# Kernel tuning notes

Measured on AMD Instinct MI355X. Metric: run time of the kernel, lower is better.

Reference implementation:

```python
import jax, jax.numpy as jnp
import numpy as np

B, C, LQ, D = 4096, 64, 32, 128
H = 192  # 1.5 * dim
MARGIN = 1.0
EPS = 1e-12


def l2norm(x):
    return x * jax.lax.rsqrt(jnp.maximum(jnp.sum(x * x, axis=1, keepdims=True), EPS))


def setup_inputs() -> dict:
    key = jax.random.key(0)
    ks = jax.random.split(key, 16)
    question_word_embs = jax.random.normal(ks[0], (B, LQ, D), jnp.float32)
    question_lengths = jax.random.randint(ks[1], (B,), 1, LQ + 1, jnp.int32)
    header_embs = jax.random.normal(ks[2], (B, C, D), jnp.float32)
    table_word_embs = jax.random.normal(ks[3], (B, C, D), jnp.float32)
    num_cols = jax.random.randint(ks[4], (B,), 1, C + 1, jnp.int32)
    masks = (jnp.arange(C)[None, :] < num_cols[:, None]).astype(jnp.float32)
    labels = (jax.random.uniform(ks[5], (B,)) < 0.5).astype(jnp.float32)
    # table_encoder_dense: Dense(1.5*dim, relu) -> Dense(dim, relu)
    W1 = jax.random.normal(ks[6], (2 * D, H), jnp.float32) / np.sqrt(2 * D)
    b1 = jnp.zeros((H,), jnp.float32)
    W2 = jax.random.normal(ks[7], (H, D), jnp.float32) / np.sqrt(H)
    b2 = jnp.zeros((D,), jnp.float32)
    # query LSTM(dim, activation='relu'): gate order i, f, c, o (Keras)
    Wx = jax.random.normal(ks[8], (D, 4 * D), jnp.float32) / np.sqrt(D)
    Wh = jax.random.normal(ks[9], (D, 4 * D), jnp.float32) / np.sqrt(D)
    b_lstm = jnp.zeros((4 * D,), jnp.float32)
    return dict(question_word_embs=question_word_embs, question_lengths=question_lengths,
                header_embs=header_embs, table_word_embs=table_word_embs,
                num_cols=num_cols, masks=masks, labels=labels,
                W1=W1, b1=b1, W2=W2, b2=b2, Wx=Wx, Wh=Wh, b_lstm=b_lstm)


def masked_lstm(x, lengths, Wx, Wh, b):
    # x: [B, L, D]; returns final hidden state at each row's true length
    xs = jnp.transpose(x, (1, 0, 2))  # [L, B, D]
    h0 = jnp.zeros((x.shape[0], D), x.dtype)
    c0 = jnp.zeros_like(h0)

    def step(carry, inp):
        h, c = carry
        t, x_t = inp
        z = x_t @ Wx + h @ Wh + b  # [B, 4D]
        i, f, g, o = jnp.split(z, 4, axis=1)
        i = jax.nn.sigmoid(i)
        f = jax.nn.sigmoid(f)
        g = jax.nn.relu(g)           # activation='relu'
        o = jax.nn.sigmoid(o)
        c_new = f * c + i * g
        h_new = o * jax.nn.relu(c_new)
        m = (t < lengths)[:, None].astype(x_t.dtype)
        return (m * h_new + (1 - m) * h, m * c_new + (1 - m) * c), None

    (h, _), _ = jax.lax.scan(step, (h0, c0), (jnp.arange(xs.shape[0]), xs))
    return h


def reference(question_word_embs, question_lengths, header_embs, table_word_embs,
              num_cols, masks, labels, W1, b1, W2, b2, Wx, Wh, b_lstm):
    # ---- table path ----
    flat = jnp.concatenate([header_embs.reshape(-1, D), table_word_embs.reshape(-1, D)], axis=1)  # [B*C, 2D]
    h = jax.nn.relu(flat @ W1 + b1)
    te = jax.nn.relu(h @ W2 + b2).reshape(B, C, D)
    te = te * masks[:, :, None]
    te = jnp.sum(te, axis=1) / num_cols.astype(jnp.float32)[:, None]
    te = l2norm(te)
    # ---- query path (ragged-word LSTM encoder) ----
    qe = masked_lstm(question_word_embs, question_lengths, Wx, Wh, b_lstm)
    qe = l2norm(qe)
    # ---- contrastive loss ----
    d = jnp.sum(jnp.square(qe - te), axis=1)
    d_sqrt = jnp.sqrt(d)
    loss = labels * d + (1.0 - labels) * jnp.square(jnp.maximum(0.0, MARGIN - d_sqrt))
    return 0.5 * jnp.mean(loss)
```

## Files before the change

### kernel.cpp

```cpp
#include <hip/hip_runtime.h>
#include <math.h>

#define B_  4096
#define C_  64
#define LQ_ 32
#define D_  128
#define H_  192

typedef __attribute__((ext_vector_type(8))) short bf16x8;
typedef __attribute__((ext_vector_type(4))) float f32x4;

#define KEEP(x) asm volatile("" : "+v"(x))

__device__ inline unsigned cvt_pk_bf16(float lo, float hi) {
    unsigned r;
    asm("v_cvt_pk_bf16_f32 %0, %1, %2" : "=v"(r) : "v"(lo), "v"(hi));
    return r;
}
__device__ inline short f2b(float x) { return (short)(cvt_pk_bf16(x, x) & 0xffff); }
__device__ inline float sigm(float x) { return 1.f / (1.f + __expf(-x)); }

__device__ inline void wg_barrier() {
    asm volatile("s_waitcnt lgkmcnt(0)" ::: "memory");
    __builtin_amdgcn_s_barrier();
    asm volatile("" ::: "memory");
}

__global__ __launch_bounds__(256) void prep_kernel(
    const float* __restrict__ W1, const float* __restrict__ W2,
    const float* __restrict__ Wx, const float* __restrict__ Wh,
    short* __restrict__ W1T, short* __restrict__ W2T, short* __restrict__ WTl)
{
    int idx = blockIdx.x * 256 + threadIdx.x;
    if (idx < 192 * 256) {
        int j = idx >> 8, k = idx & 255;
        W1T[idx] = f2b(W1[k * H_ + j]);
    }
    if (idx < 128 * 192) {
        int j = idx / 192, k = idx - j * 192;
        W2T[idx] = f2b(W2[k * D_ + j]);
    }
    if (idx < 512 * 256) {
        int p = idx >> 8, k = idx & 255;
        int w = p >> 6, g = (p >> 4) & 3, jj = p & 15;
        int jo = g * 128 + w * 16 + jj;
        float v = (k < 128) ? Wx[k * 512 + jo] : Wh[(k - 128) * 512 + jo];
        WTl[idx] = f2b(v);
    }
}

__global__ __launch_bounds__(256, 2)
void table_kernel(
    const float* __restrict__ header, const float* __restrict__ tword,
    const float* __restrict__ masks, const int* __restrict__ num_cols,
    const short* __restrict__ W1T, const float* __restrict__ b1,
    const short* __restrict__ W2T, const float* __restrict__ b2,
    float* __restrict__ te_out)
{
    const int bb0 = blockIdx.x * 4;
    const int tid = threadIdx.x;
    const int w   = tid >> 6;
    const int l   = tid & 63;
    const int lg  = l >> 4;
    const int ln  = l & 15;

    __shared__ __align__(16) float flat32[3][16 * 256];
    __shared__ __align__(16) short h_s[16 * 192];
    __shared__ float msk_s[4][64];
    __shared__ float ncol_s[4];
    __shared__ float csum_s[4][128];
    __shared__ float redq[2][4];

    bf16x8 bw1[3][8];
    float  bias1[3][4];
    #pragma unroll
    for (int ct = 0; ct < 3; ++ct) {
        int j = w * 48 + ct * 16 + ln;
        #pragma unroll
        for (int ks = 0; ks < 8; ++ks)
            bw1[ct][ks] = *(const bf16x8*)&W1T[j * 256 + ks * 32 + lg * 8];
        #pragma unroll
        for (int reg = 0; reg < 4; ++reg)
            bias1[ct][reg] = b1[w * 48 + ct * 16 + lg * 4 + reg];
    }
    #pragma unroll
    for (int ct = 0; ct < 3; ++ct) {
        #pragma unroll
        for (int ks = 0; ks < 8; ++ks) KEEP(bw1[ct][ks]);
        #pragma unroll
        for (int reg = 0; reg < 4; ++reg) KEEP(bias1[ct][reg]);
    }

    ((float*)msk_s)[tid] = masks[(size_t)bb0 * C_ + tid];
    if (tid < 4) ncol_s[tid] = (float)num_cols[bb0 + tid];

    auto stage_issue = [&](int cc, int buf) {
        int b    = bb0 + (cc >> 2);
        int row0 = (cc & 3) * 16;
        #pragma unroll
        for (int i = 0; i < 4; ++i) {
            int r = w * 4 + i;
            int p = ((l * 16) ^ ((r & 7) << 4)) >> 2;
            const float* srcp = (p < 128)
                ? header + ((size_t)b * C_ + row0 + r) * D_ + p
                : tword  + ((size_t)b * C_ + row0 + r) * D_ + (p - 128);
            __builtin_amdgcn_global_load_lds(
                (const __attribute__((address_space(1))) unsigned*)srcp,
                (__attribute__((address_space(3))) unsigned*)&flat32[buf][r * 256],
                16, 0, 0);
        }
    };

    stage_issue(0, 0);
    stage_issue(1, 1);
    __syncthreads();

    float csum[2][4] = {{0.f, 0.f, 0.f, 0.f}, {0.f, 0.f, 0.f, 0.f}};
    const int swz = (ln & 7) << 4;

    #pragma unroll 1
    for (int cc = 0; cc < 16; ++cc) {
        const int bi = cc >> 2;

        bf16x8 w2f[2][6];
        #pragma unroll
        for (int ct = 0; ct < 2; ++ct)
            #pragma unroll
            for (int ks = 0; ks < 6; ++ks)
                w2f[ct][ks] = *(const bf16x8*)&W2T[(w * 32 + ct * 16 + ln) * 192 + ks * 32 + lg * 8];
        float4 b2v[2];
        #pragma unroll
        for (int ct = 0; ct < 2; ++ct)
            b2v[ct] = *(const float4*)&b2[w * 32 + ct * 16 + lg * 4];
        if (cc + 2 < 16) stage_issue(cc + 2, (cc + 2) % 3);

        {
            const char* fb = (const char*)flat32[cc % 3] + ln * 1024;
            f32x4 acc[3];
            #pragma unroll
            for (int ct = 0; ct < 3; ++ct)
                acc[ct] = (f32x4){bias1[ct][0], bias1[ct][1], bias1[ct][2], bias1[ct][3]};
            #pragma unroll
            for (int ks = 0; ks < 8; ++ks) {
                int base = ks * 128 + lg * 32;
                f32x4 a0 = *(const f32x4*)(fb + ((base)      ^ swz));
                f32x4 a1 = *(const f32x4*)(fb + ((base + 16) ^ swz));
                unsigned uu[4];
                uu[0] = cvt_pk_bf16(a0[0], a0[1]);
                uu[1] = cvt_pk_bf16(a0[2], a0[3]);
                uu[2] = cvt_pk_bf16(a1[0], a1[1]);
                uu[3] = cvt_pk_bf16(a1[2], a1[3]);
                bf16x8 bfrag = *(bf16x8*)uu;
                #pragma unroll
                for (int ct = 0; ct < 3; ++ct)
                    acc[ct] = __builtin_amdgcn_mfma_f32_16x16x32_bf16(bw1[ct][ks], bfrag, acc[ct], 0, 0, 0);
            }
            #pragma unroll
            for (int ct = 0; ct < 3; ++ct) {
                int col0 = w * 48 + ct * 16 + lg * 4;
                uint2 hp;
                hp.x = cvt_pk_bf16(fmaxf(acc[ct][0], 0.f), fmaxf(acc[ct][1], 0.f));
                hp.y = cvt_pk_bf16(fmaxf(acc[ct][2], 0.f), fmaxf(acc[ct][3], 0.f));
                *(uint2*)((char*)h_s + ln * 384 + ((col0 * 2) ^ swz)) = hp;
            }
        }
        wg_barrier();

        {
            f32x4 acc2[2];
            #pragma unroll
            for (int ct = 0; ct < 2; ++ct)
                acc2[ct] = (f32x4){b2v[ct].x, b2v[ct].y, b2v[ct].z, b2v[ct].w};
            #pragma unroll
            for (int ks = 0; ks < 6; ++ks) {
                bf16x8 a = *(const bf16x8*)((char*)h_s + ln * 384 + ((ks * 64 + lg * 16) ^ swz));
                #pragma unroll
                for (int ct = 0; ct < 2; ++ct)
                    acc2[ct] = __builtin_amdgcn_mfma_f32_16x16x32_bf16(w2f[ct][ks], a, acc2[ct], 0, 0, 0);
            }
            float m = msk_s[bi][(cc & 3) * 16 + ln];
            #pragma unroll
            for (int ct = 0; ct < 2; ++ct)
                #pragma unroll
                for (int reg = 0; reg < 4; ++reg)
                    csum[ct][reg] = fmaf(fmaxf(acc2[ct][reg], 0.f), m, csum[ct][reg]);
        }

        if ((cc & 3) == 3) {
            #pragma unroll
            for (int s = 1; s < 16; s <<= 1)
                #pragma unroll
                for (int ct = 0; ct < 2; ++ct)
                    #pragma unroll
                    for (int reg = 0; reg < 4; ++reg)
                        csum[ct][reg] += __shfl_xor(csum[ct][reg], s, 64);
            if (ln == 0) {
                #pragma unroll
                for (int ct = 0; ct < 2; ++ct)
                    #pragma unroll
                    for (int reg = 0; reg < 4; ++reg)
                        csum_s[bi][w * 32 + ct * 16 + lg * 4 + reg] = csum[ct][reg];
            }
            #pragma unroll
            for (int ct = 0; ct < 2; ++ct)
                #pragma unroll
                for (int reg = 0; reg < 4; ++reg)
                    csum[ct][reg] = 0.f;
        }

        if (cc < 14) {
            asm volatile("s_waitcnt vmcnt(4) lgkmcnt(0)" ::: "memory");
            __builtin_amdgcn_s_barrier();
            asm volatile("" ::: "memory");
        } else if (cc == 14) {
            asm volatile("s_waitcnt vmcnt(0) lgkmcnt(0)" ::: "memory");
            __builtin_amdgcn_s_barrier();
            asm volatile("" ::: "memory");
        }
    }

    __syncthreads();
    if (tid < 128) {
        float vv[4];
        #pragma unroll
        for (int bi = 0; bi < 4; ++bi) {
            float v = csum_s[bi][tid] / ncol_s[bi];
            vv[bi] = v;
            float s2 = v * v;
            #pragma unroll
            for (int sh = 1; sh < 64; sh <<= 1) s2 += __shfl_xor(s2, sh, 64);
            if (l == 0) redq[w][bi] = s2;
        }
        __builtin_amdgcn_s_barrier();
        #pragma unroll
        for (int bi = 0; bi < 4; ++bi) {
            float inv = rsqrtf(fmaxf(redq[0][bi] + redq[1][bi], 1e-12f));
            te_out[(size_t)(bb0 + bi) * D_ + tid] = vv[bi] * inv;
        }
    }
}

__global__ __launch_bounds__(512) __attribute__((amdgpu_waves_per_eu(1, 2)))
void lstm_kernel(
    const float* __restrict__ q, const int* __restrict__ lengths,
    const short* __restrict__ WTl, const float* __restrict__ bl,
    float* __restrict__ qe_out)
{
    const int tid = threadIdx.x;
    const int b0  = blockIdx.x * 16;
    const int w   = tid >> 6;
    const int l   = tid & 63;
    const int lg  = l >> 4;
    const int ln  = l & 15;
    const int d0  = w * 16 + lg * 4;

    __shared__ __align__(16) short xh[2][16 * 256];
    __shared__ float red8[8][16];

    bf16x8 wf[4][8];
    #pragma unroll
    for (int g = 0; g < 4; ++g)
        #pragma unroll
        for (int ks = 0; ks < 8; ++ks)
            wf[g][ks] = *(const bf16x8*)&WTl[(w * 64 + g * 16 + ln) * 256 + ks * 32 + lg * 8];
    float bias[4][4];
    #pragma unroll
    for (int g = 0; g < 4; ++g)
        #pragma unroll
        for (int reg = 0; reg < 4; ++reg)
            bias[g][reg] = bl[g * 128 + d0 + reg];
    #pragma unroll
    for (int g = 0; g < 4; ++g) {
        #pragma unroll
        for (int ks = 0; ks < 8; ++ks) KEEP(wf[g][ks]);
        #pragma unroll
        for (int reg = 0; reg < 4; ++reg) KEEP(bias[g][reg]);
    }

    float creg[4] = {0.f, 0.f, 0.f, 0.f};
    float hreg[4] = {0.f, 0.f, 0.f, 0.f};
    const int len = lengths[b0 + ln];
    const int sr = tid >> 5, sc = tid & 31;

    float4 qv = *(const float4*)&q[((size_t)(b0 + sr) * LQ_ + 0) * D_ + sc * 4];

    for (int t = 0; t < LQ_; ++t) {
        char* buf = (char*)xh[t & 1];
        uint2 px; px.x = cvt_pk_bf16(qv.x, qv.y); px.y = cvt_pk_bf16(qv.z, qv.w);
        *(uint2*)(buf + sr * 512 + ((sc * 8) ^ ((sr & 7) << 4))) = px;
        uint2 ph; ph.x = cvt_pk_bf16(hreg[0], hreg[1]); ph.y = cvt_pk_bf16(hreg[2], hreg[3]);
        *(uint2*)(buf + ln * 512 + ((256 + d0 * 2) ^ ((ln & 7) << 4))) = ph;
        if (t + 1 < LQ_)
            qv = *(const float4*)&q[((size_t)(b0 + sr) * LQ_ + (t + 1)) * D_ + sc * 4];
        wg_barrier();

        f32x4 acc[4];
        #pragma unroll
        for (int g = 0; g < 4; ++g)
            acc[g] = (f32x4){bias[g][0], bias[g][1], bias[g][2], bias[g][3]};
        #pragma unroll
        for (int ks = 0; ks < 8; ++ks) {
            bf16x8 xf = *(const bf16x8*)(buf + ln * 512 + ((ks * 64 + lg * 16) ^ ((ln & 7) << 4)));
            #pragma unroll
            for (int g = 0; g < 4; ++g)
                acc[g] = __builtin_amdgcn_mfma_f32_16x16x32_bf16(wf[g][ks], xf, acc[g], 0, 0, 0);
        }

        bool live = (t < len);
        #pragma unroll
        for (int reg = 0; reg < 4; ++reg) {
            float iv = sigm(acc[0][reg]);
            float fv = sigm(acc[1][reg]);
            float gv = fmaxf(acc[2][reg], 0.f);
            float ov = sigm(acc[3][reg]);
            float cn = fmaf(fv, creg[reg], iv * gv);
            float hn = ov * fmaxf(cn, 0.f);
            if (live) { creg[reg] = cn; hreg[reg] = hn; }
        }
    }

    float sq = 0.f;
    #pragma unroll
    for (int reg = 0; reg < 4; ++reg) sq = fmaf(hreg[reg], hreg[reg], sq);
    sq += __shfl_xor(sq, 16, 64);
    sq += __shfl_xor(sq, 32, 64);
    if (l < 16) red8[w][ln] = sq;
    wg_barrier();
    float tot = 0.f;
    #pragma unroll
    for (int ww = 0; ww < 8; ++ww) tot += red8[ww][ln];
    float inv = rsqrtf(fmaxf(tot, 1e-12f));
    float4 o;
    o.x = hreg[0] * inv; o.y = hreg[1] * inv; o.z = hreg[2] * inv; o.w = hreg[3] * inv;
    *(float4*)&qe_out[(size_t)(b0 + ln) * D_ + d0] = o;
}

__global__ __launch_bounds__(64) void loss_kernel(
    const float* __restrict__ te, const float* __restrict__ qe,
    const float* __restrict__ labels, float* __restrict__ partial)
{
    const int tid = threadIdx.x;
    const int b   = blockIdx.x * 64 + tid;
    float dsum = 0.f;
    #pragma unroll 8
    for (int k4 = 0; k4 < 32; ++k4) {
        float4 a = *(const float4*)&qe[(size_t)b * D_ + k4 * 4];
        float4 c = *(const float4*)&te[(size_t)b * D_ + k4 * 4];
        float dx = a.x - c.x, dy = a.y - c.y, dz = a.z - c.z, dw = a.w - c.w;
        dsum += dx * dx + dy * dy + dz * dz + dw * dw;
    }
    float lab = labels[b];
    float ds  = sqrtf(dsum);
    float ml  = fmaxf(0.f, 1.f - ds);
    float loss = lab * dsum + (1.f - lab) * ml * ml;
    #pragma unroll
    for (int s = 32; s > 0; s >>= 1) loss += __shfl_xor(loss, s, 64);
    if (tid == 0) partial[blockIdx.x] = loss;
}

__global__ void final_kernel(const float* __restrict__ partial, float* __restrict__ out)
{
    const int tid = threadIdx.x;
    float v = partial[tid];
    #pragma unroll
    for (int s = 32; s > 0; s >>= 1) v += __shfl_xor(v, s, 64);
    if (tid == 0) out[0] = 0.5f * v / (float)B_;
}

extern "C" void kernel_launch(void* const* d_in, const int* in_sizes, int n_in,
                              void* d_out, int out_size, void* d_ws, size_t ws_size,
                              hipStream_t stream)
{
    const float* q      = (const float*)d_in[0];
    const int*   qlen   = (const int*)d_in[1];
    const float* header = (const float*)d_in[2];
    const float* tword  = (const float*)d_in[3];
    const int*   ncols  = (const int*)d_in[4];
    const float* masks  = (const float*)d_in[5];
    const float* labels = (const float*)d_in[6];
    const float* W1     = (const float*)d_in[7];
    const float* b1     = (const float*)d_in[8];
    const float* W2     = (const float*)d_in[9];
    const float* b2     = (const float*)d_in[10];
    const float* Wx     = (const float*)d_in[11];
    const float* Wh     = (const float*)d_in[12];
    const float* bl     = (const float*)d_in[13];
    float* out = (float*)d_out;

    float* te      = (float*)d_ws;
    float* qe      = te + (size_t)B_ * D_;
    float* partial = qe + (size_t)B_ * D_;
    short* W1T     = (short*)(partial + 64);
    short* W2T     = W1T + 192 * 256;
    short* WTl     = W2T + 128 * 192;

    prep_kernel<<<512, 256, 0, stream>>>(W1, W2, Wx, Wh, W1T, W2T, WTl);
    table_kernel<<<B_ / 4, 256, 0, stream>>>(header, tword, masks, ncols, W1T, b1, W2T, b2, te);
    lstm_kernel<<<B_ / 16, 512, 0, stream>>>(q, qlen, WTl, bl, qe);
    loss_kernel<<<B_ / 64, 64, 0, stream>>>(te, qe, labels, partial);
    final_kernel<<<1, 64, 0, stream>>>(partial, out);
}
```

Before: 152.5 us.

## Restructure table kernel: 16 batches per 512-thread block, bf16 LDS staging via registers

The table encoder kernel now uses 512-thread blocks, each processing 16 batch rows, one full 64-column batch per iteration. Inputs are prefetched into registers and converted to bf16 before being written to a double-buffered, swizzled LDS tile. This replaces the async global-to-LDS fp32 copies and removes the per-fragment conversions from the MFMA loop. W2 fragments and bias are now held in registers for the whole kernel instead of being reloaded every chunk. The aim is to amortise weight loads and cut LDS traffic, at the cost of more register pressure, a larger LDS footprint and fewer, larger blocks.

```diff
diff --git a/kernel.cpp b/kernel.cpp
--- a/kernel.cpp
+++ b/kernel.cpp
@@ -49,7 +49,7 @@
     }
 }
 
-__global__ __launch_bounds__(256, 2)
+__global__ __launch_bounds__(512) __attribute__((amdgpu_waves_per_eu(2, 2)))
 void table_kernel(
     const float* __restrict__ header, const float* __restrict__ tword,
     const float* __restrict__ masks, const int* __restrict__ num_cols,
@@ -57,32 +57,41 @@
     const short* __restrict__ W2T, const float* __restrict__ b2,
     float* __restrict__ te_out)
 {
-    const int bb0 = blockIdx.x * 4;
+    const int bb0 = blockIdx.x * 16;
     const int tid = threadIdx.x;
     const int w   = tid >> 6;
     const int l   = tid & 63;
     const int lg  = l >> 4;
     const int ln  = l & 15;
-
-    __shared__ __align__(16) float flat32[3][16 * 256];
-    __shared__ __align__(16) short h_s[16 * 192];
-    __shared__ float msk_s[4][64];
-    __shared__ float ncol_s[4];
-    __shared__ float csum_s[4][128];
-    __shared__ float redq[2][4];
+    const int rh  = w >> 2;
+    const int wc  = w & 3;
+
+    __shared__ __align__(16) short flat_s[2][64 * 256];
+    __shared__ __align__(16) short h_s[64 * 192];
+    __shared__ float msk_s[16][64];
+    __shared__ float ncol_s[16];
+    __shared__ float csum_s[16][128];
+    __shared__ float redq[2][16];
 
     bf16x8 bw1[3][8];
     float  bias1[3][4];
     #pragma unroll
     for (int ct = 0; ct < 3; ++ct) {
-        int j = w * 48 + ct * 16 + ln;
+        int j = wc * 48 + ct * 16 + ln;
         #pragma unroll
         for (int ks = 0; ks < 8; ++ks)
             bw1[ct][ks] = *(const bf16x8*)&W1T[j * 256 + ks * 32 + lg * 8];
         #pragma unroll
         for (int reg = 0; reg < 4; ++reg)
-            bias1[ct][reg] = b1[w * 48 + ct * 16 + lg * 4 + reg];
-    }
+            bias1[ct][reg] = b1[wc * 48 + ct * 16 + lg * 4 + reg];
+    }
+    bf16x8 w2p[6];
+    #pragma unroll
+    for (int ks = 0; ks < 6; ++ks)
+        w2p[ks] = *(const bf16x8*)&W2T[(w * 16 + ln) * 192 + ks * 32 + lg * 8];
+    float bias2[4];
+    #pragma unroll
+    for (int reg = 0; reg < 4; ++reg) bias2[reg] = b2[w * 16 + lg * 4 + reg];
     #pragma unroll
     for (int ct = 0; ct < 3; ++ct) {
         #pragma unroll
@@ -90,140 +99,119 @@
         #pragma unroll
         for (int reg = 0; reg < 4; ++reg) KEEP(bias1[ct][reg]);
     }
-
-    ((float*)msk_s)[tid] = masks[(size_t)bb0 * C_ + tid];
-    if (tid < 4) ncol_s[tid] = (float)num_cols[bb0 + tid];
-
-    auto stage_issue = [&](int cc, int buf) {
-        int b    = bb0 + (cc >> 2);
-        int row0 = (cc & 3) * 16;
-        #pragma unroll
-        for (int i = 0; i < 4; ++i) {
-            int r = w * 4 + i;
-            int p = ((l * 16) ^ ((r & 7) << 4)) >> 2;
-            const float* srcp = (p < 128)
-                ? header + ((size_t)b * C_ + row0 + r) * D_ + p
-                : tword  + ((size_t)b * C_ + row0 + r) * D_ + (p - 128);
-            __builtin_amdgcn_global_load_lds(
-                (const __attribute__((address_space(1))) unsigned*)srcp,
-                (__attribute__((address_space(3))) unsigned*)&flat32[buf][r * 256],
-                16, 0, 0);
+    #pragma unroll
+    for (int ks = 0; ks < 6; ++ks) KEEP(w2p[ks]);
+    #pragma unroll
+    for (int reg = 0; reg < 4; ++reg) KEEP(bias2[reg]);
+
+    *(float2*)&((float*)msk_s)[tid * 2] =
+        *(const float2*)&masks[(size_t)bb0 * C_ + tid * 2];
+    if (tid < 16) ncol_s[tid] = (float)num_cols[bb0 + tid];
+
+    float4 pf[8];
+    auto issue = [&](int b) {
+        #pragma unroll
+        for (int i = 0; i < 8; ++i) {
+            int slot = i * 512 + tid;
+            int r    = slot >> 6;
+            int c    = slot & 63;
+            const float* src = (c < 32)
+                ? &header[((size_t)(bb0 + b) * C_ + r) * D_ + c * 4]
+                : &tword [((size_t)(bb0 + b) * C_ + r) * D_ + (c - 32) * 4];
+            pf[i] = *(const float4*)src;
         }
     };
-
-    stage_issue(0, 0);
-    stage_issue(1, 1);
+    auto stage_write = [&](char* fbuf) {
+        #pragma unroll
+        for (int i = 0; i < 8; ++i) {
+            int slot = i * 512 + tid;
+            int r    = slot >> 6;
+            int c    = slot & 63;
+            uint2 p;
+            p.x = cvt_pk_bf16(pf[i].x, pf[i].y);
+            p.y = cvt_pk_bf16(pf[i].z, pf[i].w);
+            *(uint2*)(fbuf + r * 512 + ((c * 8) ^ ((r & 7) << 4))) = p;
+        }
+    };
+
+    issue(0);
+    stage_write((char*)flat_s[0]);
+    issue(1);
     __syncthreads();
 
-    float csum[2][4] = {{0.f, 0.f, 0.f, 0.f}, {0.f, 0.f, 0.f, 0.f}};
-    const int swz = (ln & 7) << 4;
+    float csum[4] = {0.f, 0.f, 0.f, 0.f};
 
     #pragma unroll 1
-    for (int cc = 0; cc < 16; ++cc) {
-        const int bi = cc >> 2;
-
-        bf16x8 w2f[2][6];
-        #pragma unroll
-        for (int ct = 0; ct < 2; ++ct)
-            #pragma unroll
-            for (int ks = 0; ks < 6; ++ks)
-                w2f[ct][ks] = *(const bf16x8*)&W2T[(w * 32 + ct * 16 + ln) * 192 + ks * 32 + lg * 8];
-        float4 b2v[2];
-        #pragma unroll
-        for (int ct = 0; ct < 2; ++ct)
-            b2v[ct] = *(const float4*)&b2[w * 32 + ct * 16 + lg * 4];
-        if (cc + 2 < 16) stage_issue(cc + 2, (cc + 2) % 3);
-
-        {
-            const char* fb = (const char*)flat32[cc % 3] + ln * 1024;
+    for (int b = 0; b < 16; ++b) {
+        char* fbuf = (char*)flat_s[b & 1];
+
+        #pragma unroll
+        for (int rt = 0; rt < 2; ++rt) {
+            int row = rh * 32 + rt * 16 + ln;
+            int sz  = (row & 7) << 4;
             f32x4 acc[3];
             #pragma unroll
             for (int ct = 0; ct < 3; ++ct)
                 acc[ct] = (f32x4){bias1[ct][0], bias1[ct][1], bias1[ct][2], bias1[ct][3]};
             #pragma unroll
             for (int ks = 0; ks < 8; ++ks) {
-                int base = ks * 128 + lg * 32;
-                f32x4 a0 = *(const f32x4*)(fb + ((base)      ^ swz));
-                f32x4 a1 = *(const f32x4*)(fb + ((base + 16) ^ swz));
-                unsigned uu[4];
-                uu[0] = cvt_pk_bf16(a0[0], a0[1]);
-                uu[1] = cvt_pk_bf16(a0[2], a0[3]);
-                uu[2] = cvt_pk_bf16(a1[0], a1[1]);
-                uu[3] = cvt_pk_bf16(a1[2], a1[3]);
-                bf16x8 bfrag = *(bf16x8*)uu;
+                bf16x8 xf = *(const bf16x8*)(fbuf + row * 512 + ((ks * 64 + lg * 16) ^ sz));
                 #pragma unroll
                 for (int ct = 0; ct < 3; ++ct)
-                    acc[ct] = __builtin_amdgcn_mfma_f32_16x16x32_bf16(bw1[ct][ks], bfrag, acc[ct], 0, 0, 0);
+                    acc[ct] = __builtin_amdgcn_mfma_f32_16x16x32_bf16(bw1[ct][ks], xf, acc[ct], 0, 0, 0);
             }
             #pragma unroll
             for (int ct = 0; ct < 3; ++ct) {
-                int col0 = w * 48 + ct * 16 + lg * 4;
+                int col0 = wc * 48 + ct * 16 + lg * 4;
                 uint2 hp;
                 hp.x = cvt_pk_bf16(fmaxf(acc[ct][0], 0.f), fmaxf(acc[ct][1], 0.f));
                 hp.y = cvt_pk_bf16(fmaxf(acc[ct][2], 0.f), fmaxf(acc[ct][3], 0.f));
-                *(uint2*)((char*)h_s + ln * 384 + ((col0 * 2) ^ swz)) = hp;
+                *(uint2*)((char*)h_s + row * 384 + ((col0 * 2) ^ sz)) = hp;
             }
         }
+
+        if (b < 15) {
+            stage_write((char*)flat_s[(b + 1) & 1]);
+            if (b < 14) issue(b + 2);
+        }
         wg_barrier();
 
-        {
-            f32x4 acc2[2];
-            #pragma unroll
-            for (int ct = 0; ct < 2; ++ct)
-                acc2[ct] = (f32x4){b2v[ct].x, b2v[ct].y, b2v[ct].z, b2v[ct].w};
+        #pragma unroll
+        for (int rt = 0; rt < 4; ++rt) {
+            int row = rt * 16 + ln;
+            int sz  = (row & 7) << 4;
+            f32x4 acc2 = (f32x4){bias2[0], bias2[1], bias2[2], bias2[3]};
             #pragma unroll
             for (int ks = 0; ks < 6; ++ks) {
-                bf16x8 a = *(const bf16x8*)((char*)h_s + ln * 384 + ((ks * 64 + lg * 16) ^ swz));
-                #pragma unroll
-                for (int ct = 0; ct < 2; ++ct)
-                    acc2[ct] = __builtin_amdgcn_mfma_f32_16x16x32_bf16(w2f[ct][ks], a, acc2[ct], 0, 0, 0);
+                bf16x8 hf = *(const bf16x8*)((char*)h_s + row * 384 + ((ks * 64 + lg * 16) ^ sz));
+                acc2 = __builtin_amdgcn_mfma_f32_16x16x32_bf16(w2p[ks], hf, acc2, 0, 0, 0);
             }
-            float m = msk_s[bi][(cc & 3) * 16 + ln];
-            #pragma unroll
-            for (int ct = 0; ct < 2; ++ct)
-                #pragma unroll
-                for (int reg = 0; reg < 4; ++reg)
-                    csum[ct][reg] = fmaf(fmaxf(acc2[ct][reg], 0.f), m, csum[ct][reg]);
-        }
-
-        if ((cc & 3) == 3) {
-            #pragma unroll
-            for (int s = 1; s < 16; s <<= 1)
-                #pragma unroll
-                for (int ct = 0; ct < 2; ++ct)
-                    #pragma unroll
-                    for (int reg = 0; reg < 4; ++reg)
-                        csum[ct][reg] += __shfl_xor(csum[ct][reg], s, 64);
-            if (ln == 0) {
-                #pragma unroll
-                for (int ct = 0; ct < 2; ++ct)
-                    #pragma unroll
-                    for (int reg = 0; reg < 4; ++reg)
-                        csum_s[bi][w * 32 + ct * 16 + lg * 4 + reg] = csum[ct][reg];
-            }
-            #pragma unroll
-            for (int ct = 0; ct < 2; ++ct)
-                #pragma unroll
-                for (int reg = 0; reg < 4; ++reg)
-                    csum[ct][reg] = 0.f;
-        }
-
-        if (cc < 14) {
-            asm volatile("s_waitcnt vmcnt(4) lgkmcnt(0)" ::: "memory");
-            __builtin_amdgcn_s_barrier();
-            asm volatile("" ::: "memory");
-        } else if (cc == 14) {
-            asm volatile("s_waitcnt vmcnt(0) lgkmcnt(0)" ::: "memory");
-            __builtin_amdgcn_s_barrier();
-            asm volatile("" ::: "memory");
-        }
-    }
-
-    __syncthreads();
+            float m = msk_s[b][row];
+            #pragma unroll
+            for (int reg = 0; reg < 4; ++reg)
+                csum[reg] = fmaf(fmaxf(acc2[reg], 0.f), m, csum[reg]);
+        }
+
+        #pragma unroll
+        for (int s = 1; s < 16; s <<= 1)
+            #pragma unroll
+            for (int reg = 0; reg < 4; ++reg)
+                csum[reg] += __shfl_xor(csum[reg], s, 64);
+        if (ln == 0) {
+            #pragma unroll
+            for (int reg = 0; reg < 4; ++reg)
+                csum_s[b][w * 16 + lg * 4 + reg] = csum[reg];
+        }
+        #pragma unroll
+        for (int reg = 0; reg < 4; ++reg) csum[reg] = 0.f;
+
+        wg_barrier();
+    }
+
+    float vv[16];
     if (tid < 128) {
-        float vv[4];
-        #pragma unroll
-        for (int bi = 0; bi < 4; ++bi) {
+        #pragma unroll
+        for (int bi = 0; bi < 16; ++bi) {
             float v = csum_s[bi][tid] / ncol_s[bi];
             vv[bi] = v;
             float s2 = v * v;
@@ -231,9 +219,11 @@
             for (int sh = 1; sh < 64; sh <<= 1) s2 += __shfl_xor(s2, sh, 64);
             if (l == 0) redq[w][bi] = s2;
         }
-        __builtin_amdgcn_s_barrier();
-        #pragma unroll
-        for (int bi = 0; bi < 4; ++bi) {
+    }
+    __syncthreads();
+    if (tid < 128) {
+        #pragma unroll
+        for (int bi = 0; bi < 16; ++bi) {
             float inv = rsqrtf(fmaxf(redq[0][bi] + redq[1][bi], 1e-12f));
             te_out[(size_t)(bb0 + bi) * D_ + tid] = vv[bi] * inv;
         }
@@ -395,7 +385,7 @@
     short* WTl     = W2T + 128 * 192;
 
     prep_kernel<<<512, 256, 0, stream>>>(W1, W2, Wx, Wh, W1T, W2T, WTl);
-    table_kernel<<<B_ / 4, 256, 0, stream>>>(header, tword, masks, ncols, W1T, b1, W2T, b2, te);
+    table_kernel<<<B_ / 16, 512, 0, stream>>>(header, tword, masks, ncols, W1T, b1, W2T, b2, te);
     lstm_kernel<<<B_ / 16, 512, 0, stream>>>(q, qlen, WTl, bl, qe);
     loss_kernel<<<B_ / 64, 64, 0, stream>>>(te, qe, labels, partial);
     final_kernel<<<1, 64, 0, stream>>>(partial, out);
```

Result: no change. 154.4 us (+1.3%).
